# Kernel optimization log

Hardware: AMD Instinct MI355X
Metric: run time of the kernel (lower is better)

The kernel has to match this reference:

```python
import jax, jax.numpy as jnp
import numpy as np
from jax import lax

MEM_STEPS = 3
B, T, U = 128, 512, 256
EMB = 256


def setup_inputs() -> dict:
    key = jax.random.key(0)
    ks = jax.random.split(key, 12)
    s = lambda k, shp, fan: jax.random.normal(k, shp, jnp.float32) * (1.0 / np.sqrt(fan))
    return {
        "facts": jax.random.normal(ks[0], (B, T, U), jnp.float32),
        "question": jax.random.normal(ks[1], (B, U), jnp.float32),
        "l1_W": s(ks[2], (4 * U, EMB), 4 * U),
        "l1_b": jnp.zeros((EMB,), jnp.float32),
        "l2_W": s(ks[3], (EMB, 1), EMB),
        "l2_b": jnp.zeros((1,), jnp.float32),
        "Wr": s(ks[4], (U, U), U),
        "Ur": s(ks[5], (U, U), U),
        "br": jnp.zeros((U,), jnp.float32),
        "Wh": s(ks[6], (U, U), U),
        "Uh": s(ks[7], (U, U), U),
        "bh": jnp.zeros((U,), jnp.float32),
        "mem_W": s(ks[8], (3 * U, U), 3 * U),
        "mem_b": jnp.zeros((U,), jnp.float32),
    }


def _attn_gru(facts, att, Wr, Ur, br, Wh, Uh, bh):
    # Attention-gated GRU (DMN): update gate replaced by softmax attention g_t.
    # Precompute input projections for all timesteps at once (batched GEMM).
    xr = jnp.einsum('btu,uv->btv', facts, Wr) + br  # [B,T,U]
    xh = jnp.einsum('btu,uv->btv', facts, Wh) + bh  # [B,T,U]
    h0 = jnp.zeros((facts.shape[0], Wr.shape[1]), facts.dtype)

    def step(h, inp):
        xr_t, xh_t, g_t = inp  # [B,U], [B,U], [B]
        r = jax.nn.sigmoid(xr_t + h @ Ur)
        h_tilde = jnp.tanh(xh_t + (r * h) @ Uh)
        g = g_t[:, None]
        h_new = g * h_tilde + (1.0 - g) * h
        return h_new, None

    hT, _ = lax.scan(step, h0, (xr.transpose(1, 0, 2), xh.transpose(1, 0, 2), att.T))
    return hT  # [B,U] (return_sequences=False)


def reference(facts, question, l1_W, l1_b, l2_W, l2_b, Wr, Ur, br, Wh, Uh, bh, mem_W, mem_b):
    memory = question
    for _ in range(MEM_STEPS):
        q = question[:, None, :]
        m = memory[:, None, :]
        # z: [B,T,4U] feature vector per fact
        z = jnp.concatenate([facts * q, facts * m,
                             jnp.abs(facts - q), jnp.abs(facts - m)], axis=-1)
        scores = jnp.tanh(jnp.einsum('btf,fe->bte', z, l1_W) + l1_b)
        scores = (jnp.einsum('bte,eo->bto', scores, l2_W) + l2_b)[..., 0]  # [B,T]
        att = jax.nn.softmax(scores, axis=1)  # softmax over facts
        episode = _attn_gru(facts, att, Wr, Ur, br, Wh, Uh, bh)  # [B,U]
        memory = jax.nn.relu(jnp.concatenate([memory, episode, question], axis=1) @ mem_W + mem_b)
    return jnp.concatenate([memory, question], axis=1)  # [B, 2U]
```

## Files before the change

kernel.cpp:

```cpp
#include <hip/hip_runtime.h>


#define DEVI static __device__ __forceinline__

typedef float f32x4 __attribute__((ext_vector_type(4)));
typedef unsigned short u16x8 __attribute__((ext_vector_type(8)));
typedef unsigned int u32x4 __attribute__((ext_vector_type(4)));
typedef __bf16 bf16x8 __attribute__((ext_vector_type(8)));

DEVI f32x4 mfma16(u16x8 a, u16x8 b, f32x4 c) {
  return __builtin_amdgcn_mfma_f32_16x16x32_bf16(
      __builtin_bit_cast(bf16x8, a), __builtin_bit_cast(bf16x8, b), c, 0, 0, 0);
}
DEVI float bf2f(unsigned short u) {
  unsigned int x = ((unsigned int)u) << 16;
  return __builtin_bit_cast(float, x);
}
DEVI float lo2f(unsigned int u) {
  unsigned int x = u << 16;
  return __builtin_bit_cast(float, x);
}
DEVI float hi2f(unsigned int u) {
  unsigned int x = u & 0xffff0000u;
  return __builtin_bit_cast(float, x);
}
DEVI unsigned short f2bf(float f) {
  unsigned int u = __builtin_bit_cast(unsigned int, f);
  return (unsigned short)((u + 0x7fffu + ((u >> 16) & 1u)) >> 16);
}
DEVI unsigned int cvtpk(float lo, float hi) {
  unsigned int r;
  asm("v_cvt_pk_bf16_f32 %0, %1, %2" : "=v"(r) : "v"(lo), "v"(hi));
  return r;
}
DEVI float sigmoid_f(float x) {
  float e = __expf(-x);
  return __builtin_amdgcn_rcpf(1.f + e);
}
DEVI float tanh_f(float x) {
  float xc = fmaxf(x, -12.f);
  float e = __expf(-2.f * xc);
  return (1.f - e) * __builtin_amdgcn_rcpf(1.f + e);
}
DEVI int invperm(int s) { return 32 * (s >> 5) + 16 * (s & 1) + ((s & 31) >> 1); }


__global__ void cast_facts_kernel(const float* __restrict__ in,
                                  unsigned short* __restrict__ out, int n8) {
  int i = blockIdx.x * blockDim.x + threadIdx.x;
  int stride = gridDim.x * blockDim.x;
  for (; i < n8; i += stride) {
    const float4* p = (const float4*)(in + (size_t)i * 8);
    float4 a = p[0], b = p[1];
    u16x8 o;
    o[0] = f2bf(a.x); o[1] = f2bf(a.y); o[2] = f2bf(a.z); o[3] = f2bf(a.w);
    o[4] = f2bf(b.x); o[5] = f2bf(b.y); o[6] = f2bf(b.z); o[7] = f2bf(b.w);
    *(u16x8*)(out + (size_t)i * 8) = o;
  }
}

__global__ void prep_weights_kernel(const float* __restrict__ Wr,
                                    const float* __restrict__ Wh,
                                    const float* __restrict__ Ur,
                                    const float* __restrict__ Uh,
                                    const float* __restrict__ l1W,
                                    const float* __restrict__ br,
                                    const float* __restrict__ bh,
                                    const float* __restrict__ memW,
                                    unsigned short* __restrict__ wrT,
                                    unsigned short* __restrict__ whT,
                                    unsigned short* __restrict__ urT,
                                    unsigned short* __restrict__ uhT,
                                    unsigned short* __restrict__ l1qT,
                                    unsigned short* __restrict__ l1mT,
                                    unsigned short* __restrict__ memWT,
                                    float* __restrict__ brP,
                                    float* __restrict__ bhP) {
  int z = blockIdx.y;
  int r = blockIdx.x;
  int c = threadIdx.x;
  if (z < 2) {
    const float* src = (z == 0) ? Wr : Wh;
    unsigned short* dst = (z == 0) ? wrT : whT;
    dst[r * 256 + c] = f2bf(src[c * 256 + invperm(r)]);
    if (r == 0) {
      if (z == 0) brP[c] = br[invperm(c)];
      else        bhP[c] = bh[invperm(c)];
    }
  } else if (z < 4) {
    const float* src = (z == 2) ? Ur : Uh;
    unsigned short* dst = (z == 2) ? urT : uhT;
    dst[r * 256 + c] = f2bf(src[invperm(c) * 256 + invperm(r)]);
  } else if (z < 6) {
    unsigned short* dst = (z == 4) ? l1qT : l1mT;
    for (int kk = c; kk < 512; kk += 256) {
      int srow;
      if (z == 4) srow = (kk < 256) ? kk : (kk + 256);
      else        srow = (kk < 256) ? (kk + 256) : (kk + 512);
      dst[r * 512 + kk] = f2bf(l1W[srow * 256 + r]);
    }
  } else {
    for (int kk = c; kk < 768; kk += 256) {
      int ksrc = (kk < 256) ? kk : (kk < 512 ? 256 + invperm(kk - 256) : kk);
      memWT[r * 768 + kk] = f2bf(memW[ksrc * 256 + r]);
    }
  }
}

__global__ void init_qm_kernel(const float* __restrict__ question,
                               unsigned short* __restrict__ qbf,
                               unsigned short* __restrict__ mbf) {
  int i = blockIdx.x * 256 + threadIdx.x;
  unsigned short u = f2bf(question[i]);
  qbf[i] = u;
  mbf[i] = u;
}

__global__ __launch_bounds__(256, 2) void gemm_xrxh_kernel(
    const unsigned short* __restrict__ factsb,
    const unsigned short* __restrict__ wrT,
    const unsigned short* __restrict__ whT,
    const float* __restrict__ brP, const float* __restrict__ bhP,
    unsigned short* __restrict__ xrxh) {
  const int b = blockIdx.x >> 3;
  const int t0 = (blockIdx.x & 7) * 64;
  const int w = threadIdx.x >> 6, l = threadIdx.x & 63;
  const int l15 = l & 15, lg = l >> 4;
  const int koff = lg * 8;
  const int m0 = t0 + w * 16;

  f32x4 accR[16], accH[16];
  const f32x4 zz = {0.f, 0.f, 0.f, 0.f};
#pragma unroll
  for (int nt = 0; nt < 16; nt++) { accR[nt] = zz; accH[nt] = zz; }

  const unsigned short* arow = factsb + ((size_t)b * 512 + (m0 + l15)) * 256;
#pragma unroll
  for (int ks = 0; ks < 8; ks++) {
    u16x8 a = *(const u16x8*)&arow[ks * 32 + koff];
#pragma unroll
    for (int nt = 0; nt < 16; nt++) {
      u16x8 bwr = *(const u16x8*)&wrT[(size_t)(nt * 16 + l15) * 256 + ks * 32 + koff];
      u16x8 bwh = *(const u16x8*)&whT[(size_t)(nt * 16 + l15) * 256 + ks * 32 + koff];
      accR[nt] = mfma16(a, bwr, accR[nt]);
      accH[nt] = mfma16(a, bwh, accH[nt]);
    }
  }
#pragma unroll
  for (int nt = 0; nt < 16; nt++) {
    const int col = nt * 16 + l15;
    const float bvr = brP[col], bvh = bhP[col];
#pragma unroll
    for (int r = 0; r < 4; r++) {
      const int t = m0 + lg * 4 + r;
      unsigned int pk = cvtpk(accR[nt][r] + bvr, accH[nt][r] + bvh);
      *(unsigned int*)&xrxh[((size_t)t * 128 + b) * 512 + col * 2] = pk;
    }
  }
}

__global__ __launch_bounds__(256, 2) void scores_kernel(
    const unsigned short* __restrict__ factsb,
    const unsigned short* __restrict__ l1qT,
    const unsigned short* __restrict__ l1mT,
    const float* __restrict__ l1b,
    const unsigned short* __restrict__ qbf,
    const unsigned short* __restrict__ mbf,
    const float* __restrict__ l2w, float* __restrict__ scores) {
  const int b = blockIdx.x >> 2;
  const int t0 = (blockIdx.x & 2) * 64;
  const int half = blockIdx.x & 1;
  const int w = threadIdx.x >> 6, l = threadIdx.x & 63;
  const int l15 = l & 15, lg = l >> 4;
  const int koff = lg * 8;
  const int tbase = (blockIdx.x & 3) * 128;
  (void)t0; (void)half;
  const int m0 = tbase + w * 16;

  f32x4 acc[2][16];
  const f32x4 zz = {0.f, 0.f, 0.f, 0.f};
#pragma unroll
  for (int s = 0; s < 2; s++)
#pragma unroll
    for (int nt = 0; nt < 16; nt++) acc[s][nt] = zz;

  const unsigned short* arow0 = factsb + ((size_t)b * 512 + (m0 + l15)) * 256;
  const unsigned short* arow1 = arow0 + 64 * 256;
  const unsigned short* qv = qbf + b * 256;
  const unsigned short* mv = mbf + b * 256;

  for (int q2 = 0; q2 < 4; q2++) {
    const unsigned short* WTs = (q2 & 1) ? l1mT : l1qT;
    const unsigned short* vvp = (q2 & 1) ? mv : qv;
    const int bko = (q2 >> 1) * 256;
    const bool isabs = (q2 >= 2);
#pragma unroll
    for (int kss = 0; kss < 8; kss++) {
      u32x4 f0 = *(const u32x4*)&arow0[kss * 32 + koff];
      u32x4 f1 = *(const u32x4*)&arow1[kss * 32 + koff];
      u32x4 vv = *(const u32x4*)&vvp[kss * 32 + koff];
      u32x4 a0, a1;
#pragma unroll
      for (int j = 0; j < 4; j++) {
        float vl = lo2f(vv[j]), vh = hi2f(vv[j]);
        if (isabs) {
          a0[j] = cvtpk(lo2f(f0[j]) - vl, hi2f(f0[j]) - vh) & 0x7fff7fffu;
          a1[j] = cvtpk(lo2f(f1[j]) - vl, hi2f(f1[j]) - vh) & 0x7fff7fffu;
        } else {
          a0[j] = cvtpk(lo2f(f0[j]) * vl, hi2f(f0[j]) * vh);
          a1[j] = cvtpk(lo2f(f1[j]) * vl, hi2f(f1[j]) * vh);
        }
      }
      u16x8 ab0 = __builtin_bit_cast(u16x8, a0);
      u16x8 ab1 = __builtin_bit_cast(u16x8, a1);
#pragma unroll
      for (int nt = 0; nt < 16; nt++) {
        u16x8 bb = *(const u16x8*)&WTs[(size_t)(nt * 16 + l15) * 512 + bko + kss * 32 + koff];
        acc[0][nt] = mfma16(ab0, bb, acc[0][nt]);
        acc[1][nt] = mfma16(ab1, bb, acc[1][nt]);
      }
    }
  }

  float part[2][4] = {{0.f, 0.f, 0.f, 0.f}, {0.f, 0.f, 0.f, 0.f}};
#pragma unroll
  for (int nt = 0; nt < 16; nt++) {
    const int col = nt * 16 + l15;
    const float lw = l2w[col];
    const float bv = l1b[col];
#pragma unroll
    for (int s = 0; s < 2; s++)
#pragma unroll
      for (int r = 0; r < 4; r++) part[s][r] += tanh_f(acc[s][nt][r] + bv) * lw;
  }
#pragma unroll
  for (int m = 1; m < 16; m <<= 1)
#pragma unroll
    for (int s = 0; s < 2; s++)
#pragma unroll
      for (int r = 0; r < 4; r++) part[s][r] += __shfl_xor(part[s][r], m, 64);
  if (l15 == 0) {
#pragma unroll
    for (int s = 0; s < 2; s++)
#pragma unroll
      for (int r = 0; r < 4; r++)
        scores[(size_t)b * 512 + m0 + s * 64 + lg * 4 + r] = part[s][r];
  }
}

__global__ void softmax_kernel(const float* __restrict__ scores,
                               float* __restrict__ att) {
  int b = blockIdx.x;
  int l = threadIdx.x;
  float v[8];
#pragma unroll
  for (int i = 0; i < 8; i++) v[i] = scores[b * 512 + l * 8 + i];
  float mx = v[0];
#pragma unroll
  for (int i = 1; i < 8; i++) mx = fmaxf(mx, v[i]);
#pragma unroll
  for (int m = 1; m < 64; m <<= 1) mx = fmaxf(mx, __shfl_xor(mx, m, 64));
  float s = 0.f;
#pragma unroll
  for (int i = 0; i < 8; i++) { v[i] = __expf(v[i] - mx); s += v[i]; }
#pragma unroll
  for (int m = 1; m < 64; m <<= 1) s += __shfl_xor(s, m, 64);
  float inv = __builtin_amdgcn_rcpf(s);
#pragma unroll
  for (int i = 0; i < 8; i++) att[(l * 8 + i) * 128 + b] = v[i] * inv;
}

struct PF {
  uint2 x[4];
  f32x4 g;
};

__global__ __launch_bounds__(512, 2) void scan_kernel(
    const unsigned short* __restrict__ xrxh,
    const float* __restrict__ att,
    const unsigned short* __restrict__ urT,
    const unsigned short* __restrict__ uhT,
    const unsigned short* __restrict__ memWT,
    const float* __restrict__ memb,
    const unsigned short* __restrict__ qbf,
    unsigned short* __restrict__ mbf,
    float* __restrict__ memory)
{
  constexpr int PAD = 264;
  constexpr int CPAD = 776;
  __shared__ unsigned short hlds[16 * PAD];
  __shared__ unsigned short rhlds[16 * PAD];
  __shared__ unsigned short cat[16 * CPAD];
  const int w = threadIdx.x >> 6, l = threadIdx.x & 63;
  const int l15 = l & 15, lg = l >> 4;
  const int koff = lg * 8;
  const int b0 = blockIdx.x * 16;
  const int lb = lg * 4;

  u16x8 urf[2][8], uhf[2][8];
#pragma unroll
  for (int q = 0; q < 2; q++) {
    const int sc = 32 * w + 2 * l15 + q;
#pragma unroll
    for (int ks = 0; ks < 8; ks++) {
      urf[q][ks] = *(const u16x8*)&urT[sc * 256 + ks * 32 + koff];
      uhf[q][ks] = *(const u16x8*)&uhT[sc * 256 + ks * 32 + koff];
    }
  }
  for (int i = threadIdx.x; i < 16 * PAD; i += 512) hlds[i] = 0;
  __syncthreads();

  const int hread = l15 * PAD + koff;
  int wdw[4], ro[4];
#pragma unroll
  for (int r = 0; r < 4; r++) {
    wdw[r] = (lb + r) * (PAD / 2) + 16 * w + l15;
    ro[r] = (b0 + lb + r) * 512 + 64 * w + 4 * l15;
  }
  const int attoff = b0 + lb;

  float hc[2][4];
#pragma unroll
  for (int q = 0; q < 2; q++)
#pragma unroll
    for (int r = 0; r < 4; r++) hc[q][r] = 0.f;

  const f32x4 zz = {0.f, 0.f, 0.f, 0.f};

  auto prefetch = [&](int t) {
    PF pf;
    const unsigned short* xb = xrxh + (size_t)t * 65536;
#pragma unroll
    for (int r = 0; r < 4; r++) pf.x[r] = *(const uint2*)&xb[ro[r]];
    pf.g = *(const f32x4*)&att[t * 128 + attoff];
    return pf;
  };

  auto step = [&](const PF& pf) {
    u16x8 hf[8];
#pragma unroll
    for (int ks = 0; ks < 8; ks++)
      hf[ks] = *(const u16x8*)&hlds[hread + ks * 32];
    f32x4 aA[2] = {zz, zz}, aB[2] = {zz, zz};
#pragma unroll
    for (int ks = 0; ks < 4; ks++)
#pragma unroll
      for (int q = 0; q < 2; q++) {
        aA[q] = mfma16(hf[ks], urf[q][ks], aA[q]);
        aB[q] = mfma16(hf[ks + 4], urf[q][ks + 4], aB[q]);
      }
#pragma unroll
    for (int r = 0; r < 4; r++) {
      const uint2 xv = pf.x[r];
      float s0 = aA[0][r] + aB[0][r] + lo2f(xv.x);
      float s1 = aA[1][r] + aB[1][r] + lo2f(xv.y);
      float rh0 = sigmoid_f(s0) * hc[0][r];
      float rh1 = sigmoid_f(s1) * hc[1][r];
      ((unsigned int*)rhlds)[wdw[r]] = cvtpk(rh0, rh1);
    }
    __syncthreads();
    u16x8 rf[8];
#pragma unroll
    for (int ks = 0; ks < 8; ks++)
      rf[ks] = *(const u16x8*)&rhlds[hread + ks * 32];
    f32x4 bA[2] = {zz, zz}, bB[2] = {zz, zz};
#pragma unroll
    for (int ks = 0; ks < 4; ks++)
#pragma unroll
      for (int q = 0; q < 2; q++) {
        bA[q] = mfma16(rf[ks], uhf[q][ks], bA[q]);
        bB[q] = mfma16(rf[ks + 4], uhf[q][ks + 4], bB[q]);
      }
#pragma unroll
    for (int r = 0; r < 4; r++) {
      const uint2 xv = pf.x[r];
      float ht0 = tanh_f(bA[0][r] + bB[0][r] + hi2f(xv.x));
      float ht1 = tanh_f(bA[1][r] + bB[1][r] + hi2f(xv.y));
      const float g = pf.g[r];
      hc[0][r] = fmaf(g, ht0 - hc[0][r], hc[0][r]);
      hc[1][r] = fmaf(g, ht1 - hc[1][r], hc[1][r]);
      ((unsigned int*)hlds)[wdw[r]] = cvtpk(hc[0][r], hc[1][r]);
    }
    __syncthreads();
  };

  PF cur = prefetch(0);
#pragma unroll 2
  for (int t = 0; t < 512; t++) {
    PF nxt = prefetch(t + 1);
    step(cur);
    cur = nxt;
  }

  {
    const int i = (int)threadIdx.x;
    const int bb = i >> 5, cc = (i & 31) * 8;
    *(u16x8*)&cat[bb * CPAD + cc] = *(const u16x8*)&mbf[(b0 + bb) * 256 + cc];
    *(u16x8*)&cat[bb * CPAD + 512 + cc] = *(const u16x8*)&qbf[(b0 + bb) * 256 + cc];
  }
#pragma unroll
  for (int r = 0; r < 4; r++) {
    *(unsigned int*)&cat[(lb + r) * CPAD + 256 + 32 * w + 2 * l15] =
        cvtpk(hc[0][r], hc[1][r]);
  }
  __syncthreads();

  f32x4 mA[2] = {zz, zz}, mB[2] = {zz, zz};
#pragma unroll
  for (int ks = 0; ks < 24; ks += 2) {
    u16x8 a0 = *(const u16x8*)&cat[l15 * CPAD + ks * 32 + koff];
    u16x8 a1 = *(const u16x8*)&cat[l15 * CPAD + (ks + 1) * 32 + koff];
#pragma unroll
    for (int q = 0; q < 2; q++) {
      const int vrow = (2 * w + q) * 16 + l15;
      u16x8 bf0 = *(const u16x8*)&memWT[(size_t)vrow * 768 + ks * 32 + koff];
      u16x8 bf1 = *(const u16x8*)&memWT[(size_t)vrow * 768 + (ks + 1) * 32 + koff];
      mA[q] = mfma16(a0, bf0, mA[q]);
      mB[q] = mfma16(a1, bf1, mB[q]);
    }
  }
#pragma unroll
  for (int q = 0; q < 2; q++) {
    const int col = (2 * w + q) * 16 + l15;
    const float bv = memb[col];
#pragma unroll
    for (int r = 0; r < 4; r++) {
      float v = fmaxf(mA[q][r] + mB[q][r] + bv, 0.f);
      memory[(size_t)(b0 + lb + r) * 256 + col] = v;
      mbf[(size_t)(b0 + lb + r) * 256 + col] = f2bf(v);
    }
  }
}

__global__ void writeout_kernel(const float* __restrict__ memory,
                                const float* __restrict__ question,
                                float* __restrict__ out) {
  int i = blockIdx.x * 256 + threadIdx.x;
  int b = i >> 9, c = i & 511;
  out[i] = (c < 256) ? memory[b * 256 + c] : question[b * 256 + (c - 256)];
}

extern "C" void kernel_launch(void* const* d_in, const int* in_sizes, int n_in,
                              void* d_out, int out_size, void* d_ws, size_t ws_size,
                              hipStream_t stream) {
  (void)in_sizes; (void)n_in; (void)out_size; (void)ws_size;
  const float* facts = (const float*)d_in[0];
  const float* question = (const float*)d_in[1];
  const float* l1W = (const float*)d_in[2];
  const float* l1b = (const float*)d_in[3];
  const float* l2W = (const float*)d_in[4];
  const float* Wr = (const float*)d_in[6];
  const float* Ur = (const float*)d_in[7];
  const float* br = (const float*)d_in[8];
  const float* Wh = (const float*)d_in[9];
  const float* Uh = (const float*)d_in[10];
  const float* bh = (const float*)d_in[11];
  const float* memW = (const float*)d_in[12];
  const float* memb = (const float*)d_in[13];
  float* out = (float*)d_out;

  char* ws = (char*)d_ws;
  unsigned short* factsb = (unsigned short*)(ws + 0);
  unsigned short* xrxh   = (unsigned short*)(ws + 33554432);
  unsigned short* wrT    = (unsigned short*)(ws + 100663296);
  unsigned short* whT    = (unsigned short*)(ws + 100794368);
  unsigned short* urT    = (unsigned short*)(ws + 100925440);
  unsigned short* uhT    = (unsigned short*)(ws + 101056512);
  unsigned short* l1qT   = (unsigned short*)(ws + 101187584);
  unsigned short* l1mT   = (unsigned short*)(ws + 101711872);
  unsigned short* qbf    = (unsigned short*)(ws + 102236160);
  unsigned short* mbf    = (unsigned short*)(ws + 102301696);
  float* scores          = (float*)(ws + 102367232);
  float* att             = (float*)(ws + 102629376);
  float* memory          = (float*)(ws + 102891520);
  float* brP             = (float*)(ws + 103022592);
  float* bhP             = (float*)(ws + 103023616);
  unsigned short* memWT  = (unsigned short*)(ws + 103024640);

  cast_facts_kernel<<<2048, 256, 0, stream>>>(facts, factsb, 2097152);
  prep_weights_kernel<<<dim3(256, 7), 256, 0, stream>>>(
      Wr, Wh, Ur, Uh, l1W, br, bh, memW,
      wrT, whT, urT, uhT, l1qT, l1mT, memWT, brP, bhP);
  init_qm_kernel<<<128, 256, 0, stream>>>(question, qbf, mbf);

  gemm_xrxh_kernel<<<1024, 256, 0, stream>>>(factsb, wrT, whT, brP, bhP, xrxh);

  for (int step = 0; step < 3; step++) {
    scores_kernel<<<512, 256, 0, stream>>>(factsb, l1qT, l1mT, l1b, qbf, mbf, l2W, scores);
    softmax_kernel<<<128, 64, 0, stream>>>(scores, att);
    scan_kernel<<<8, 512, 0, stream>>>(xrxh, att, urT, uhT, memWT, memb, qbf, mbf, memory);
  }
  writeout_kernel<<<256, 256, 0, stream>>>(memory, question, out);
}
```

Measured before the change: 2.496 ms.

## Precompute question-dependent scores GEMM half once and reuse across memory steps

The l1 GEMM over z splits into question-dependent terms (facts*q, |facts-q|) and memory-dependent terms. Within one call the question terms are the same for all three steps, so they are now computed once, stored as bf16 accumulator fragments in workspace, and reloaded as the starting accumulators each step. This halves the MFMA work per step in exchange for an extra 32 MB write and three 32 MB reads, plus bf16 rounding of partial sums. The scan kernel's LDS row padding is also changed from 264 to 262.

```diff
diff --git a/kernel.cpp b/kernel.cpp
--- a/kernel.cpp
+++ b/kernel.cpp
@@ -159,6 +159,7 @@
   }
 }
 
+template <int SMODE>
 __global__ __launch_bounds__(256, 2) void scores_kernel(
     const unsigned short* __restrict__ factsb,
     const unsigned short* __restrict__ l1qT,
@@ -166,30 +167,42 @@
     const float* __restrict__ l1b,
     const unsigned short* __restrict__ qbf,
     const unsigned short* __restrict__ mbf,
-    const float* __restrict__ l2w, float* __restrict__ scores) {
+    const float* __restrict__ l2w, float* __restrict__ scores,
+    uint2* __restrict__ accQ) {
   const int b = blockIdx.x >> 2;
-  const int t0 = (blockIdx.x & 2) * 64;
-  const int half = blockIdx.x & 1;
   const int w = threadIdx.x >> 6, l = threadIdx.x & 63;
   const int l15 = l & 15, lg = l >> 4;
   const int koff = lg * 8;
   const int tbase = (blockIdx.x & 3) * 128;
-  (void)t0; (void)half;
   const int m0 = tbase + w * 16;
+  const int fragbase = ((blockIdx.x * 4 + w) * 2) * 16;
 
   f32x4 acc[2][16];
   const f32x4 zz = {0.f, 0.f, 0.f, 0.f};
-#pragma unroll
-  for (int s = 0; s < 2; s++)
-#pragma unroll
-    for (int nt = 0; nt < 16; nt++) acc[s][nt] = zz;
+  if constexpr (SMODE == 2) {
+#pragma unroll
+    for (int s = 0; s < 2; s++)
+#pragma unroll
+      for (int nt = 0; nt < 16; nt++) {
+        uint2 v = accQ[(size_t)(fragbase + s * 16 + nt) * 64 + l];
+        acc[s][nt][0] = lo2f(v.x); acc[s][nt][1] = hi2f(v.x);
+        acc[s][nt][2] = lo2f(v.y); acc[s][nt][3] = hi2f(v.y);
+      }
+  } else {
+#pragma unroll
+    for (int s = 0; s < 2; s++)
+#pragma unroll
+      for (int nt = 0; nt < 16; nt++) acc[s][nt] = zz;
+  }
 
   const unsigned short* arow0 = factsb + ((size_t)b * 512 + (m0 + l15)) * 256;
   const unsigned short* arow1 = arow0 + 64 * 256;
   const unsigned short* qv = qbf + b * 256;
   const unsigned short* mv = mbf + b * 256;
 
-  for (int q2 = 0; q2 < 4; q2++) {
+  const int nq = (SMODE == 0) ? 4 : 2;
+  for (int qi = 0; qi < nq; qi++) {
+    const int q2 = (SMODE == 0) ? qi : (SMODE == 1) ? 2 * qi : 2 * qi + 1;
     const unsigned short* WTs = (q2 & 1) ? l1mT : l1qT;
     const unsigned short* vvp = (q2 & 1) ? mv : qv;
     const int bko = (q2 >> 1) * 256;
@@ -222,6 +235,19 @@
     }
   }
 
+  if constexpr (SMODE == 1) {
+#pragma unroll
+    for (int s = 0; s < 2; s++)
+#pragma unroll
+      for (int nt = 0; nt < 16; nt++) {
+        uint2 v;
+        v.x = cvtpk(acc[s][nt][0], acc[s][nt][1]);
+        v.y = cvtpk(acc[s][nt][2], acc[s][nt][3]);
+        accQ[(size_t)(fragbase + s * 16 + nt) * 64 + l] = v;
+      }
+    return;
+  }
+
   float part[2][4] = {{0.f, 0.f, 0.f, 0.f}, {0.f, 0.f, 0.f, 0.f}};
 #pragma unroll
   for (int nt = 0; nt < 16; nt++) {
@@ -286,7 +312,7 @@
     unsigned short* __restrict__ mbf,
     float* __restrict__ memory)
 {
-  constexpr int PAD = 264;
+  constexpr int PAD = 262;
   constexpr int CPAD = 776;
   __shared__ unsigned short hlds[16 * PAD];
   __shared__ unsigned short rhlds[16 * PAD];
@@ -443,7 +469,7 @@
 extern "C" void kernel_launch(void* const* d_in, const int* in_sizes, int n_in,
                               void* d_out, int out_size, void* d_ws, size_t ws_size,
                               hipStream_t stream) {
-  (void)in_sizes; (void)n_in; (void)out_size; (void)ws_size;
+  (void)in_sizes; (void)n_in; (void)out_size;
   const float* facts = (const float*)d_in[0];
   const float* question = (const float*)d_in[1];
   const float* l1W = (const float*)d_in[2];
@@ -476,6 +502,8 @@
   float* brP             = (float*)(ws + 103022592);
   float* bhP             = (float*)(ws + 103023616);
   unsigned short* memWT  = (unsigned short*)(ws + 103024640);
+  uint2* accQ            = (uint2*)(ws + 103417856);
+  const bool split = ws_size >= 103417856ull + 33554432ull;
 
   cast_facts_kernel<<<2048, 256, 0, stream>>>(facts, factsb, 2097152);
   prep_weights_kernel<<<dim3(256, 7), 256, 0, stream>>>(
@@ -484,9 +512,17 @@
   init_qm_kernel<<<128, 256, 0, stream>>>(question, qbf, mbf);
 
   gemm_xrxh_kernel<<<1024, 256, 0, stream>>>(factsb, wrT, whT, brP, bhP, xrxh);
+  if (split)
+    scores_kernel<1><<<512, 256, 0, stream>>>(factsb, l1qT, l1mT, l1b, qbf, mbf,
+                                              l2W, scores, accQ);
 
   for (int step = 0; step < 3; step++) {
-    scores_kernel<<<512, 256, 0, stream>>>(factsb, l1qT, l1mT, l1b, qbf, mbf, l2W, scores);
+    if (split)
+      scores_kernel<2><<<512, 256, 0, stream>>>(factsb, l1qT, l1mT, l1b, qbf, mbf,
+                                                l2W, scores, accQ);
+    else
+      scores_kernel<0><<<512, 256, 0, stream>>>(factsb, l1qT, l1mT, l1b, qbf, mbf,
+                                                l2W, scores, accQ);
     softmax_kernel<<<128, 64, 0, stream>>>(scores, att);
     scan_kernel<<<8, 512, 0, stream>>>(xrxh, att, urT, uhT, memWT, memb, qbf, mbf, memory);
   }
```

New measurement: 2.972 ms. 19.1% more time.
